# Kernel optimization log

Measured on AMD Instinct MI355X. Metric: run time of the kernel, lower is better.

The kernel has to match this reference:

```python
import jax, jax.numpy as jnp
import numpy as np

D = 128; DFF = 256; NH = 4; HD = D // NH
B = 8; T = 1024
PAIRS = [(0, 1), (1, 2), (0, 2)]  # (ABSTRACT,DYNAMIC),(DYNAMIC,CONCRETE),(ABSTRACT,CONCRETE)
BW = 0.5 / 3.0   # bridge_weight / len(BRIDGE_PAIRS)
LB_W = 0.01


def _hex_np():
    # itertools.product([-1,1], repeat=6): index i = 6-bit binary of i, MSB first, 0->-1
    bits = (np.arange(64)[:, None] >> np.arange(5, -1, -1)) & 1
    return (bits * 2.0 - 1.0).astype(np.float32)


def _anchors_np():
    h = _hex_np()
    idx = {'GEO': 0, 'HYDRO': 18, 'PYRO': 45, 'AERO': 6, 'COSMO': 27, 'NOOS': 63}
    a = (h[idx['NOOS']] + h[idx['COSMO']]) / 2.0   # ABSTRACT
    d = (h[idx['AERO']] + h[idx['PYRO']]) / 2.0    # DYNAMIC
    c = (h[idx['GEO']] + h[idx['HYDRO']]) / 2.0    # CONCRETE
    return np.stack([a, d, c]).astype(np.float32)


def _ln(x, g, b, eps=1e-5):
    m = x.mean(-1, keepdims=True)
    v = ((x - m) ** 2).mean(-1, keepdims=True)
    return (x - m) * jax.lax.rsqrt(v + eps) * g + b


def _mha(q, kv, in_w, out_w):
    # torch nn.MultiheadAttention, bias=False, batch_first
    Bq, Tq, _ = q.shape
    wq, wk, wv = in_w[:D], in_w[D:2 * D], in_w[2 * D:]
    Q = (q @ wq.T).reshape(Bq, Tq, NH, HD)
    K = (kv @ wk.T).reshape(Bq, Tq, NH, HD)
    V = (kv @ wv.T).reshape(Bq, Tq, NH, HD)
    scores = jnp.einsum('bqhd,bkhd->bhqk', Q, K) / jnp.sqrt(jnp.float32(HD))
    attn = jax.nn.softmax(scores, axis=-1)
    o = jnp.einsum('bhqk,bkhd->bqhd', attn, V).reshape(Bq, Tq, D)
    return o @ out_w.T


def setup_inputs() -> dict:
    key = jax.random.key(0)
    ks = iter(jax.random.split(key, 40))
    r = lambda shape, s=0.02: jax.random.normal(next(ks), shape, dtype=jnp.float32) * s
    return {
        'x': jax.random.normal(next(ks), (B, T, D), dtype=jnp.float32),
        'gr_norm_g': jnp.ones((D,), jnp.float32), 'gr_norm_b': jnp.zeros((D,), jnp.float32),
        'q6_w': r((6, D), 0.1),
        'log_temp': jnp.log(jnp.float32(0.5)),
        'grp_norm_g': jnp.ones((3, D), jnp.float32), 'grp_norm_b': jnp.zeros((3, D), jnp.float32),
        'grp_proj_w': r((3, 2, D), 0.1), 'grp_proj_b': jnp.zeros((3, 2), jnp.float32),
        'me_norm_g': jnp.ones((6, D), jnp.float32), 'me_norm_b': jnp.zeros((6, D), jnp.float32),
        'me_gate_w': r((6, DFF, D)), 'me_val_w': r((6, DFF, D)), 'me_out_w': r((6, D, DFF)),
        'br_in_w': r((3, 3 * D, D)), 'br_out_w': r((3, D, D)),
        'br_nq_g': jnp.ones((3, D), jnp.float32), 'br_nq_b': jnp.zeros((3, D), jnp.float32),
        'br_nkv_g': jnp.ones((3, D), jnp.float32), 'br_nkv_b': jnp.zeros((3, D), jnp.float32),
        'br_nffn_g': jnp.ones((3, D), jnp.float32), 'br_nffn_b': jnp.zeros((3, D), jnp.float32),
        'br_gate_w': r((3, 2 * D, D)), 'br_val_w': r((3, 2 * D, D)), 'br_ffn_out_w': r((3, D, 2 * D)),
        'br_gate': jnp.full((3,), -2.0, dtype=jnp.float32),
        'out_norm_g': jnp.ones((D,), jnp.float32), 'out_norm_b': jnp.zeros((D,), jnp.float32),
        'out_w': r((D, D)),
    }


def reference(x, gr_norm_g, gr_norm_b, q6_w, log_temp, grp_norm_g, grp_norm_b,
              grp_proj_w, grp_proj_b, me_norm_g, me_norm_b, me_gate_w, me_val_w,
              me_out_w, br_in_w, br_out_w, br_nq_g, br_nq_b, br_nkv_g, br_nkv_b,
              br_nffn_g, br_nffn_b, br_gate_w, br_val_w, br_ffn_out_w, br_gate,
              out_norm_g, out_norm_b, out_w):
    hexg = jnp.asarray(_hex_np())        # (64, 6)
    anchors = jnp.asarray(_anchors_np())  # (3, 6)

    # ---- GlobalRouter ----
    h = _ln(x, gr_norm_g, gr_norm_b)
    soft_bits = jnp.tanh(h @ q6_w.T)                       # (B,T,6)
    sim = soft_bits @ hexg.T                               # (B,T,64)
    temp = jnp.clip(jnp.exp(log_temp), 0.1, 5.0)
    hex_w = jax.nn.softmax(sim / temp, axis=-1)
    soft_hex = hex_w @ hexg                                # (B,T,6)
    group_weights = jax.nn.softmax(soft_hex @ anchors.T, axis=-1)  # (B,T,3)
    mw = group_weights.mean(axis=(0, 1))
    lb_total = -(mw * jnp.log(mw + 1e-8)).sum()

    # ---- all 6 micro experts (per-expert LayerNorm shares x's stats) ----
    m = x.mean(-1, keepdims=True)
    v = ((x - m) ** 2).mean(-1, keepdims=True)
    xn = (x - m) * jax.lax.rsqrt(v + 1e-5)                 # (B,T,D)
    hme = xn[None] * me_norm_g[:, None, None, :] + me_norm_b[:, None, None, :]  # (6,B,T,D)
    gate = jax.nn.silu(jnp.einsum('ebtd,efd->ebtf', hme, me_gate_w))
    val = jnp.einsum('ebtd,efd->ebtf', hme, me_val_w)
    eo = jnp.einsum('ebtf,edf->ebtd', gate * val, me_out_w)  # (6,B,T,D)

    # ---- per-group routing (2 experts each, top_k=2) ----
    group_outs = []
    for g in range(3):  # groups ordered [ABSTRACT, DYNAMIC, CONCRETE]; experts [2g, 2g+1]
        hg = xn * grp_norm_g[g] + grp_norm_b[g]
        logits = hg @ grp_proj_w[g].T + grp_proj_b[g]      # (B,T,2)
        w = jax.nn.softmax(logits, axis=-1)
        vals, idx = jax.lax.top_k(w, 2)                    # k = min(top_k=2, n=2)
        sparse = (jax.nn.one_hot(idx, 2, dtype=w.dtype) * vals[..., None]).sum(-2)
        sparse = sparse / (sparse.sum(-1, keepdims=True) + 1e-8)
        mwg = w.mean(axis=(0, 1))
        lb_total = lb_total - (mwg * jnp.log(mwg + 1e-8)).sum()
        go = sparse[..., 0:1] * eo[2 * g] + sparse[..., 1:2] * eo[2 * g + 1]
        group_outs.append(group_weights[..., g:g + 1] * go)

    # ---- bridge experts ----
    bridge_sum = jnp.zeros_like(x)
    for i, (a, b) in enumerate(PAIRS):
        xq, xk = group_outs[a], group_outs[b]
        qn = _ln(xq, br_nq_g[i], br_nq_b[i])
        kvn = _ln(xk, br_nkv_g[i], br_nkv_b[i])
        xb = xq + _mha(qn, kvn, br_in_w[i], br_out_w[i])
        hb = _ln(xb, br_nffn_g[i], br_nffn_b[i])
        ff = (jax.nn.silu(hb @ br_gate_w[i].T) * (hb @ br_val_w[i].T)) @ br_ffn_out_w[i].T
        xb = (xb + ff) * jax.nn.sigmoid(br_gate[i])
        bridge_sum = bridge_sum + BW * xb

    combined = group_outs[0] + group_outs[1] + group_outs[2] + bridge_sum
    out = _ln(combined, out_norm_g, out_norm_b) @ out_w.T
    return out, lb_total * LB_W
```

## Files before the change

kernel.cpp:

```cpp
#include <hip/hip_runtime.h>
#include <math.h>

#define DD    128
#define DFF   256
#define NHH   4
#define HDD   32
#define BB    8
#define TT    1024
#define NTOK  (BB*TT)
#define LDK   72
#define QKVN  384

#define WB_MEGATE 0
#define WB_MEVAL  196608
#define WB_MEOUT  393216
#define WB_BRIN   589824
#define WB_BROUT  737280
#define WB_BRG    786432
#define WB_BRV    884736
#define WB_BRF    983040
#define WB_OUTW   1081344
#define WB_TOT    1097728

typedef __bf16 bf16x8 __attribute__((ext_vector_type(8)));
typedef float  f32x4  __attribute__((ext_vector_type(4)));

__device__ __forceinline__ float wsum(float v){
#pragma unroll
  for(int o=32;o>0;o>>=1) v += __shfl_xor(v,o,64);
  return v;
}
__device__ __forceinline__ float wmaxr(float v){
#pragma unroll
  for(int o=32;o>0;o>>=1) v = fmaxf(v,__shfl_xor(v,o,64));
  return v;
}
__device__ __forceinline__ unsigned short f2bf(float x){
  __bf16 h = (__bf16)x;
  unsigned short u;
  __builtin_memcpy(&u, &h, 2);
  return u;
}

__device__ __forceinline__ void stage16(const float* __restrict__ gp,
                                        unsigned short* __restrict__ dst){
  float4 f0 = *reinterpret_cast<const float4*>(gp);
  float4 f1 = *reinterpret_cast<const float4*>(gp+4);
  float4 f2 = *reinterpret_cast<const float4*>(gp+8);
  float4 f3 = *reinterpret_cast<const float4*>(gp+12);
  float f[16] = {f0.x,f0.y,f0.z,f0.w, f1.x,f1.y,f1.z,f1.w,
                 f2.x,f2.y,f2.z,f2.w, f3.x,f3.y,f3.z,f3.w};
  unsigned short h[16];
#pragma unroll
  for(int j=0;j<16;j++) h[j] = f2bf(f[j]);
  *reinterpret_cast<uint4*>(dst)   = *reinterpret_cast<const uint4*>(h);
  *reinterpret_cast<uint4*>(dst+8) = *reinterpret_cast<const uint4*>(h+8);
}

__device__ __forceinline__ void stage16bf(const unsigned short* __restrict__ gp,
                                          unsigned short* __restrict__ dst){
  const uint4* s = reinterpret_cast<const uint4*>(gp);
  *reinterpret_cast<uint4*>(dst)   = s[0];
  *reinterpret_cast<uint4*>(dst+8) = s[1];
}

__device__ __forceinline__ void stageLN(const float* __restrict__ fr,
                                        float mean, float rstd,
                                        const float* __restrict__ g,
                                        const float* __restrict__ b,
                                        unsigned short* __restrict__ dst){
  unsigned short h[16];
#pragma unroll
  for(int j=0;j<16;j++){
    float y = (fr[j]-mean)*rstd*g[j] + b[j];
    h[j] = f2bf(y);
  }
  *reinterpret_cast<uint4*>(dst)   = *reinterpret_cast<const uint4*>(h);
  *reinterpret_cast<uint4*>(dst+8) = *reinterpret_cast<const uint4*>(h+8);
}

__global__ __launch_bounds__(256) void wconv(
    const float* __restrict__ a0, const float* __restrict__ a1, const float* __restrict__ a2,
    const float* __restrict__ a3, const float* __restrict__ a4, const float* __restrict__ a5,
    const float* __restrict__ a6, const float* __restrict__ a7, const float* __restrict__ a8,
    unsigned short* __restrict__ dst, float qsc){
  size_t i = ((size_t)blockIdx.x*256 + threadIdx.x)*4;
  if(i >= WB_TOT) return;
  const float* s; size_t off = i; float sc = 1.0f;
  if(i < WB_MEVAL){ s=a0; }
  else if(i < WB_MEOUT){ s=a1; off = i-WB_MEVAL; }
  else if(i < WB_BRIN ){ s=a2; off = i-WB_MEOUT; }
  else if(i < WB_BROUT){ s=a3; off = i-WB_BRIN;
    int row = (int)(off>>7); if((row % 384) < 128) sc = qsc; }
  else if(i < WB_BRG ){ s=a4; off = i-WB_BROUT; }
  else if(i < WB_BRV ){ s=a5; off = i-WB_BRG; }
  else if(i < WB_BRF ){ s=a6; off = i-WB_BRV; }
  else if(i < WB_OUTW){ s=a7; off = i-WB_BRF; }
  else { s=a8; off = i-WB_OUTW; }
  float4 v = *reinterpret_cast<const float4*>(s + off);
  unsigned short h4[4] = {f2bf(v.x*sc), f2bf(v.y*sc), f2bf(v.z*sc), f2bf(v.w*sc)};
  *reinterpret_cast<uint2*>(dst + i) = *reinterpret_cast<const uint2*>(h4);
}

__global__ __launch_bounds__(256) void routing_kernel(
    const float* __restrict__ x,
    const float* __restrict__ gr_g, const float* __restrict__ gr_b,
    const float* __restrict__ q6,   const float* __restrict__ logtemp,
    const float* __restrict__ grp_g,const float* __restrict__ grp_b,
    const float* __restrict__ gpw,  const float* __restrict__ gpb,
    float* __restrict__ gw_out, float* __restrict__ coef, float* __restrict__ part){
  __shared__ float sp[4][9];
  int lane = threadIdx.x & 63;
  int wv   = threadIdx.x >> 6;
  int t    = (blockIdx.x<<2) + wv;
  const float* xr = x + (size_t)t*DD;
  float r0 = xr[lane], r1 = xr[lane+64];
  float mn = wsum(r0+r1) * (1.0f/DD);
  float d0 = r0-mn, d1 = r1-mn;
  float vv = wsum(d0*d0 + d1*d1) * (1.0f/DD);
  float rstd = rsqrtf(vv + 1e-5f);
  float x0 = d0*rstd, x1 = d1*rstd;
  float h0 = x0*gr_g[lane]+gr_b[lane];
  float h1 = x1*gr_g[lane+64]+gr_b[lane+64];
  float sb[6];
#pragma unroll
  for(int j=0;j<6;j++){
    float p = h0*q6[j*DD+lane] + h1*q6[j*DD+lane+64];
    sb[j] = tanhf(wsum(p));
  }
  float sim = 0.f;
#pragma unroll
  for(int j=0;j<6;j++) sim += ((lane>>(5-j))&1) ? sb[j] : -sb[j];
  float temp = expf(logtemp[0]); temp = fminf(fmaxf(temp,0.1f),5.0f);
  float mx = wmaxr(sim);
  float p  = expf((sim-mx)/temp);
  float w  = p / wsum(p);
  float sh[6];
#pragma unroll
  for(int j=0;j<6;j++) sh[j] = wsum(((lane>>(5-j))&1) ? w : -w);
  const float A0[6]={0,1,1,0,1,1}, A1[6]={0,-1,0,1,0,0}, A2[6]={-1,0,-1,-1,0,-1};
  float l0=0,l1=0,l2=0;
#pragma unroll
  for(int j=0;j<6;j++){ l0+=sh[j]*A0[j]; l1+=sh[j]*A1[j]; l2+=sh[j]*A2[j]; }
  float m3 = fmaxf(l0,fmaxf(l1,l2));
  float e0=expf(l0-m3), e1=expf(l1-m3), e2=expf(l2-m3);
  float inv3 = 1.0f/(e0+e1+e2);
  float g0=e0*inv3, g1=e1*inv3, g2=e2*inv3;
  if(lane==0){ gw_out[t*3]=g0; gw_out[t*3+1]=g1; gw_out[t*3+2]=g2; }
  float gwv[3]={g0,g1,g2};
  float pw[6];
#pragma unroll
  for(int g=0; g<3; g++){
    float hg0 = x0*grp_g[g*DD+lane]    + grp_b[g*DD+lane];
    float hg1 = x1*grp_g[g*DD+lane+64] + grp_b[g*DD+lane+64];
    float q0 = wsum(hg0*gpw[(g*2+0)*DD+lane] + hg1*gpw[(g*2+0)*DD+lane+64]) + gpb[g*2+0];
    float q1 = wsum(hg0*gpw[(g*2+1)*DD+lane] + hg1*gpw[(g*2+1)*DD+lane+64]) + gpb[g*2+1];
    float mm = fmaxf(q0,q1);
    float a0 = expf(q0-mm), a1 = expf(q1-mm);
    float inv = 1.0f/(a0+a1);
    float w0 = a0*inv, w1 = a1*inv;
    pw[g*2]=w0; pw[g*2+1]=w1;
    float invs = 1.0f/(w0+w1+1e-8f);
    if(lane==0){
      coef[(size_t)(2*g  )*NTOK + t] = gwv[g]*w0*invs;
      coef[(size_t)(2*g+1)*NTOK + t] = gwv[g]*w1*invs;
    }
  }
  if(lane==0){
    sp[wv][0]=g0; sp[wv][1]=g1; sp[wv][2]=g2;
#pragma unroll
    for(int k=0;k<6;k++) sp[wv][3+k]=pw[k];
  }
  __syncthreads();
  if(threadIdx.x<9){
    part[blockIdx.x*9+threadIdx.x] =
      sp[0][threadIdx.x]+sp[1][threadIdx.x]+sp[2][threadIdx.x]+sp[3][threadIdx.x];
  }
}

__global__ __launch_bounds__(256) void lb_kernel(const float* __restrict__ part, float* __restrict__ outlb){
  __shared__ float sm[4][9];
  float acc[9] = {};
  for(int i=threadIdx.x; i<2048; i+=256){
#pragma unroll
    for(int c=0;c<9;c++) acc[c] += part[i*9+c];
  }
#pragma unroll
  for(int c=0;c<9;c++) acc[c] = wsum(acc[c]);
  int wv = threadIdx.x>>6, lane = threadIdx.x&63;
  if(lane==0){
#pragma unroll
    for(int c=0;c<9;c++) sm[wv][c]=acc[c];
  }
  __syncthreads();
  if(threadIdx.x==0){
    const float invN = 1.0f/(float)NTOK;
    float lb=0;
#pragma unroll
    for(int c=0;c<9;c++){
      float s = sm[0][c]+sm[1][c]+sm[2][c]+sm[3][c];
      float mw = s*invN;
      lb -= mw*logf(mw+1e-8f);
    }
    outlb[0] = lb*0.01f;
  }
}

template<int MODE,int LN,int ABF,int OBF,int PSEL,int RSEL,int SUM,int QKV,int MRG>
__global__ __launch_bounds__(256) void gemm_mfma(
    const void* __restrict__ Ap, const unsigned short* __restrict__ W, void* __restrict__ Cp,
    int M, int N, int K,
    const float* __restrict__ sv, const float* __restrict__ bv,
    const float* __restrict__ resid, const float* __restrict__ gptr,
    size_t az, size_t wz, size_t cz, size_t pz, size_t rz, size_t gz){
  __shared__ unsigned short As[64*LDK];
  __shared__ unsigned short Ws[64*LDK];
  const int z = blockIdx.z;
  const float* A = (const float*)Ap;
  const unsigned short* Ab = (const unsigned short*)Ap;
  if(QKV){
    bool isQ = (blockIdx.x < 2);
    int s = isQ ? ((z==1)?1:0) : ((z==0)?1:2);
    A += (size_t)s*NTOK*DD;
    if(!isQ){ sv = resid; bv = gptr; }
  } else if(PSEL==0){ A += z*az; Ab += z*az; }
  else if(PSEL==1){ int s = (z==1)?1:0; A += (size_t)s*NTOK*DD; Ab += (size_t)s*NTOK*DD; }
  else            { int s = (z==0)?1:2; A += (size_t)s*NTOK*DD; Ab += (size_t)s*NTOK*DD; }
  W += z*wz;
  float* C = (float*)Cp + z*cz;
  unsigned short* Cb = (unsigned short*)Cp + z*cz;
  const float* rs = resid;
  if(RSEL==0) rs += z*rz;
  else { int s = (z==1)?1:0; rs += (size_t)s*NTOK*DD; }
  sv += z*pz; bv += z*pz;
  const float* gp2 = gptr + z*gz;
  int tid  = threadIdx.x;
  int m0   = blockIdx.y*64, n0 = blockIdx.x*64;
  int w    = tid>>6, lane = tid&63;
  int wr   = (w>>1)*32, wc = (w&1)*32;
  int r    = tid>>2, seg = (tid&3)*16;
  f32x4 acc[2][2] = {};
  auto step = [&](){
#pragma unroll
    for(int kk=0;kk<64;kk+=32){
      int ko = kk + (lane>>4)*8;
      bf16x8 a0 = *reinterpret_cast<const bf16x8*>(&As[(wr    + (lane&15))*LDK + ko]);
      bf16x8 a1 = *reinterpret_cast<const bf16x8*>(&As[(wr+16 + (lane&15))*LDK + ko]);
      bf16x8 b0 = *reinterpret_cast<const bf16x8*>(&Ws[(wc    + (lane&15))*LDK + ko]);
      bf16x8 b1 = *reinterpret_cast<const bf16x8*>(&Ws[(wc+16 + (lane&15))*LDK + ko]);
      acc[0][0] = __builtin_amdgcn_mfma_f32_16x16x32_bf16(a0,b0,acc[0][0],0,0,0);
      acc[0][1] = __builtin_amdgcn_mfma_f32_16x16x32_bf16(a0,b1,acc[0][1],0,0,0);
      acc[1][0] = __builtin_amdgcn_mfma_f32_16x16x32_bf16(a1,b0,acc[1][0],0,0,0);
      acc[1][1] = __builtin_amdgcn_mfma_f32_16x16x32_bf16(a1,b1,acc[1][1],0,0,0);
    }
  };
  if(LN){
    float fr[32]; float mean, rstd;
    if(SUM){
#pragma unroll
      for(int j=0;j<32;j++) fr[j]=0.f;
#pragma unroll
      for(int s=0;s<3;s++){
        const float* r1 = A     + (size_t)s*NTOK*DD + (size_t)(m0+r)*K + seg;
        const float* r2 = resid + (size_t)s*NTOK*DD + (size_t)(m0+r)*K + seg;
#pragma unroll
        for(int j=0;j<4;j++){
          float4 v1 = *reinterpret_cast<const float4*>(r1 + j*4);
          float4 v2 = *reinterpret_cast<const float4*>(r2 + j*4);
          fr[j*4]+=v1.x+v2.x; fr[j*4+1]+=v1.y+v2.y; fr[j*4+2]+=v1.z+v2.z; fr[j*4+3]+=v1.w+v2.w;
          float4 w1 = *reinterpret_cast<const float4*>(r1 + 64 + j*4);
          float4 w2 = *reinterpret_cast<const float4*>(r2 + 64 + j*4);
          fr[16+j*4]+=w1.x+w2.x; fr[16+j*4+1]+=w1.y+w2.y; fr[16+j*4+2]+=w1.z+w2.z; fr[16+j*4+3]+=w1.w+w2.w;
        }
      }
    } else {
      const float* arow = A + (size_t)(m0+r)*K + seg;
#pragma unroll
      for(int j=0;j<4;j++) *reinterpret_cast<float4*>(&fr[j*4])    = *reinterpret_cast<const float4*>(arow + j*4);
#pragma unroll
      for(int j=0;j<4;j++) *reinterpret_cast<float4*>(&fr[16+j*4]) = *reinterpret_cast<const float4*>(arow + 64 + j*4);
    }
    float s1=0.f, s2=0.f;
#pragma unroll
    for(int j=0;j<32;j++){ s1 += fr[j]; s2 += fr[j]*fr[j]; }
    s1 += __shfl_xor(s1,1,64); s1 += __shfl_xor(s1,2,64);
    s2 += __shfl_xor(s2,1,64); s2 += __shfl_xor(s2,2,64);
    mean = s1*(1.0f/DD);
    float var = s2*(1.0f/DD) - mean*mean;
    rstd = rsqrtf(var + 1e-5f);
#pragma unroll
    for(int kh=0; kh<2; ++kh){
      __syncthreads();
      stageLN(fr + kh*16, mean, rstd, sv + kh*64 + seg, bv + kh*64 + seg, &As[r*LDK + seg]);
      stage16bf(W + (size_t)(n0+r)*K + kh*64 + seg, &Ws[r*LDK + seg]);
      __syncthreads();
      step();
    }
  } else if(MRG){
    const float* op0 = (const float*)Ap + (size_t)(2*z)*NTOK*DD;
    const float* op1 = op0 + (size_t)NTOK*DD;
    const float* mp = sv + (size_t)(2*z)*NTOK*NHH;
    const float* lp = bv + (size_t)(2*z)*NTOK*NHH;
    const int row = m0 + r;
#pragma unroll
    for(int kh=0; kh<2; ++kh){
      const int k0 = kh*64;
      const int hh = (k0+seg)>>5;
      size_t ix = (size_t)row*NHH + hh;
      float ma=mp[ix], mb2=mp[(size_t)NTOK*NHH+ix];
      float la=lp[ix], lb2=lp[(size_t)NTOK*NHH+ix];
      float Mx = fmaxf(ma,mb2);
      float f0 = __builtin_amdgcn_exp2f(ma-Mx), f1 = __builtin_amdgcn_exp2f(mb2-Mx);
      float inv = 1.0f/(la*f0+lb2*f1);
      f0 *= inv; f1 *= inv;
      __syncthreads();
      {
        unsigned short hbuf[16];
        size_t base = (size_t)row*DD + k0 + seg;
#pragma unroll
        for(int j=0;j<4;j++){
          float4 v0 = *reinterpret_cast<const float4*>(op0 + base + j*4);
          float4 v1 = *reinterpret_cast<const float4*>(op1 + base + j*4);
          hbuf[j*4  ] = f2bf(v0.x*f0 + v1.x*f1);
          hbuf[j*4+1] = f2bf(v0.y*f0 + v1.y*f1);
          hbuf[j*4+2] = f2bf(v0.z*f0 + v1.z*f1);
          hbuf[j*4+3] = f2bf(v0.w*f0 + v1.w*f1);
        }
        *reinterpret_cast<uint4*>(&As[r*LDK+seg])   = *reinterpret_cast<const uint4*>(hbuf);
        *reinterpret_cast<uint4*>(&As[r*LDK+seg+8]) = *reinterpret_cast<const uint4*>(hbuf+8);
      }
      stage16bf(W + (size_t)(n0+r)*K + k0 + seg, &Ws[r*LDK + seg]);
      __syncthreads();
      step();
    }
  } else {
    for(int k0=0;k0<K;k0+=64){
      __syncthreads();
      if(ABF) stage16bf(Ab + (size_t)(m0+r)*K + k0 + seg, &As[r*LDK + seg]);
      else    stage16(A  + (size_t)(m0+r)*K + k0 + seg, &As[r*LDK + seg]);
      stage16bf(W + (size_t)(n0+r)*K + k0 + seg, &Ws[r*LDK + seg]);
      __syncthreads();
      step();
    }
  }
#pragma unroll
  for(int i=0;i<2;i++){
#pragma unroll
    for(int j=0;j<2;j++){
      int mb = m0 + wr + i*16 + (lane>>4)*4;
      int n  = n0 + wc + j*16 + (lane&15);
#pragma unroll
      for(int rg=0;rg<4;rg++){
        int m = mb + rg;
        float v = acc[i][j][rg];
        size_t o = (size_t)m*N + n;
        if(MODE==0){ if(OBF) Cb[o] = f2bf(v); else C[o] = v; }
        else if(MODE==3){ C[o] = rs[o] + v; }
        else if(MODE==5){
          float gs = (0.5f/3.0f)/(1.0f+expf(-gp2[0]));
          C[o] = gs*(rs[o]+v);
        }
      }
    }
  }
}

__global__ __launch_bounds__(256) void gemm_dual(
    const float* __restrict__ A, const unsigned short* __restrict__ G,
    const unsigned short* __restrict__ V,
    unsigned short* __restrict__ C, int M, int N, int K,
    const float* __restrict__ sv, const float* __restrict__ bv,
    size_t az, size_t wz, size_t cz, size_t pz){
  __shared__ unsigned short As[64*LDK];
  __shared__ unsigned short Gs[64*LDK];
  __shared__ unsigned short Vs[64*LDK];
  const int z = blockIdx.z;
  A += z*az; G += z*wz; V += z*wz; C += z*cz; sv += z*pz; bv += z*pz;
  int tid  = threadIdx.x;
  int m0   = blockIdx.y*64, n0 = blockIdx.x*64;
  int w    = tid>>6, lane = tid&63;
  int wr   = (w>>1)*32, wc = (w&1)*32;
  int r    = tid>>2, seg = (tid&3)*16;
  f32x4 accg[2][2] = {};
  f32x4 accv[2][2] = {};
  float fr[32]; float mean, rstd;
  {
    const float* arow = A + (size_t)(m0+r)*K + seg;
#pragma unroll
    for(int j=0;j<4;j++) *reinterpret_cast<float4*>(&fr[j*4])    = *reinterpret_cast<const float4*>(arow + j*4);
#pragma unroll
    for(int j=0;j<4;j++) *reinterpret_cast<float4*>(&fr[16+j*4]) = *reinterpret_cast<const float4*>(arow + 64 + j*4);
    float s1=0.f, s2=0.f;
#pragma unroll
    for(int j=0;j<32;j++){ s1 += fr[j]; s2 += fr[j]*fr[j]; }
    s1 += __shfl_xor(s1,1,64); s1 += __shfl_xor(s1,2,64);
    s2 += __shfl_xor(s2,1,64); s2 += __shfl_xor(s2,2,64);
    mean = s1*(1.0f/DD);
    float var = s2*(1.0f/DD) - mean*mean;
    rstd = rsqrtf(var + 1e-5f);
  }
#pragma unroll
  for(int kh=0; kh<2; ++kh){
    int k0 = kh*64;
    __syncthreads();
    stageLN(fr + kh*16, mean, rstd, sv + k0 + seg, bv + k0 + seg, &As[r*LDK + seg]);
    stage16bf(G + (size_t)(n0+r)*K + k0 + seg, &Gs[r*LDK + seg]);
    stage16bf(V + (size_t)(n0+r)*K + k0 + seg, &Vs[r*LDK + seg]);
    __syncthreads();
#pragma unroll
    for(int kk=0;kk<64;kk+=32){
      int ko = kk + (lane>>4)*8;
      bf16x8 a0 = *reinterpret_cast<const bf16x8*>(&As[(wr    + (lane&15))*LDK + ko]);
      bf16x8 a1 = *reinterpret_cast<const bf16x8*>(&As[(wr+16 + (lane&15))*LDK + ko]);
      bf16x8 g0 = *reinterpret_cast<const bf16x8*>(&Gs[(wc    + (lane&15))*LDK + ko]);
      bf16x8 g1 = *reinterpret_cast<const bf16x8*>(&Gs[(wc+16 + (lane&15))*LDK + ko]);
      bf16x8 v0 = *reinterpret_cast<const bf16x8*>(&Vs[(wc    + (lane&15))*LDK + ko]);
      bf16x8 v1 = *reinterpret_cast<const bf16x8*>(&Vs[(wc+16 + (lane&15))*LDK + ko]);
      accg[0][0] = __builtin_amdgcn_mfma_f32_16x16x32_bf16(a0,g0,accg[0][0],0,0,0);
      accg[0][1] = __builtin_amdgcn_mfma_f32_16x16x32_bf16(a0,g1,accg[0][1],0,0,0);
      accg[1][0] = __builtin_amdgcn_mfma_f32_16x16x32_bf16(a1,g0,accg[1][0],0,0,0);
      accg[1][1] = __builtin_amdgcn_mfma_f32_16x16x32_bf16(a1,g1,accg[1][1],0,0,0);
      accv[0][0] = __builtin_amdgcn_mfma_f32_16x16x32_bf16(a0,v0,accv[0][0],0,0,0);
      accv[0][1] = __builtin_amdgcn_mfma_f32_16x16x32_bf16(a0,v1,accv[0][1],0,0,0);
      accv[1][0] = __builtin_amdgcn_mfma_f32_16x16x32_bf16(a1,v0,accv[1][0],0,0,0);
      accv[1][1] = __builtin_amdgcn_mfma_f32_16x16x32_bf16(a1,v1,accv[1][1],0,0,0);
    }
  }
#pragma unroll
  for(int i=0;i<2;i++){
#pragma unroll
    for(int j=0;j<2;j++){
      int mb = m0 + wr + i*16 + (lane>>4)*4;
      int n  = n0 + wc + j*16 + (lane&15);
#pragma unroll
      for(int rg=0;rg<4;rg++){
        float gg = accg[i][j][rg];
        float vv = accv[i][j][rg];
        float sg = gg/(1.0f+expf(-gg));
        C[(size_t)(mb+rg)*N + n] = f2bf(sg*vv);
      }
    }
  }
}

__global__ __launch_bounds__(256) void gemm_moe2(
    const unsigned short* __restrict__ Ab, const unsigned short* __restrict__ Wb,
    float* __restrict__ Cb, const float* __restrict__ coef){
  __shared__ unsigned short As0[64*LDK];
  __shared__ unsigned short As1[64*LDK];
  __shared__ unsigned short Ws0[64*LDK];
  __shared__ unsigned short Ws1[64*LDK];
  const int g = blockIdx.z;
  const unsigned short* A0 = Ab + (size_t)(2*g)*NTOK*DFF;
  const unsigned short* A1 = A0 + (size_t)NTOK*DFF;
  const unsigned short* W0 = Wb + (size_t)(2*g)*DD*DFF;
  const unsigned short* W1 = W0 + (size_t)DD*DFF;
  float* C = Cb + (size_t)g*NTOK*DD;
  const float* c0 = coef + (size_t)(2*g)*NTOK;
  const float* c1 = c0 + NTOK;
  int tid  = threadIdx.x;
  int m0   = blockIdx.y*64, n0 = blockIdx.x*64;
  int w    = tid>>6, lane = tid&63;
  int wr   = (w>>1)*32, wc = (w&1)*32;
  int r    = tid>>2, seg = (tid&3)*16;
  f32x4 a0acc[2][2] = {};
  f32x4 a1acc[2][2] = {};
  for(int k0=0;k0<DFF;k0+=64){
    __syncthreads();
    stage16bf(A0 + (size_t)(m0+r)*DFF + k0 + seg, &As0[r*LDK + seg]);
    stage16bf(A1 + (size_t)(m0+r)*DFF + k0 + seg, &As1[r*LDK + seg]);
    stage16bf(W0 + (size_t)(n0+r)*DFF + k0 + seg, &Ws0[r*LDK + seg]);
    stage16bf(W1 + (size_t)(n0+r)*DFF + k0 + seg, &Ws1[r*LDK + seg]);
    __syncthreads();
#pragma unroll
    for(int kk=0;kk<64;kk+=32){
      int ko = kk + (lane>>4)*8;
      bf16x8 x00 = *reinterpret_cast<const bf16x8*>(&As0[(wr    + (lane&15))*LDK + ko]);
      bf16x8 x01 = *reinterpret_cast<const bf16x8*>(&As0[(wr+16 + (lane&15))*LDK + ko]);
      bf16x8 x10 = *reinterpret_cast<const bf16x8*>(&As1[(wr    + (lane&15))*LDK + ko]);
      bf16x8 x11 = *reinterpret_cast<const bf16x8*>(&As1[(wr+16 + (lane&15))*LDK + ko]);
      bf16x8 w00 = *reinterpret_cast<const bf16x8*>(&Ws0[(wc    + (lane&15))*LDK + ko]);
      bf16x8 w01 = *reinterpret_cast<const bf16x8*>(&Ws0[(wc+16 + (lane&15))*LDK + ko]);
      bf16x8 w10 = *reinterpret_cast<const bf16x8*>(&Ws1[(wc    + (lane&15))*LDK + ko]);
      bf16x8 w11 = *reinterpret_cast<const bf16x8*>(&Ws1[(wc+16 + (lane&15))*LDK + ko]);
      a0acc[0][0] = __builtin_amdgcn_mfma_f32_16x16x32_bf16(x00,w00,a0acc[0][0],0,0,0);
      a0acc[0][1] = __builtin_amdgcn_mfma_f32_16x16x32_bf16(x00,w01,a0acc[0][1],0,0,0);
      a0acc[1][0] = __builtin_amdgcn_mfma_f32_16x16x32_bf16(x01,w00,a0acc[1][0],0,0,0);
      a0acc[1][1] = __builtin_amdgcn_mfma_f32_16x16x32_bf16(x01,w01,a0acc[1][1],0,0,0);
      a1acc[0][0] = __builtin_amdgcn_mfma_f32_16x16x32_bf16(x10,w10,a1acc[0][0],0,0,0);
      a1acc[0][1] = __builtin_amdgcn_mfma_f32_16x16x32_bf16(x10,w11,a1acc[0][1],0,0,0);
      a1acc[1][0] = __builtin_amdgcn_mfma_f32_16x16x32_bf16(x11,w10,a1acc[1][0],0,0,0);
      a1acc[1][1] = __builtin_amdgcn_mfma_f32_16x16x32_bf16(x11,w11,a1acc[1][1],0,0,0);
    }
  }
#pragma unroll
  for(int i=0;i<2;i++){
#pragma unroll
    for(int j=0;j<2;j++){
      int mb = m0 + wr + i*16 + (lane>>4)*4;
      int n  = n0 + wc + j*16 + (lane&15);
#pragma unroll
      for(int rg=0;rg<4;rg++){
        int m = mb + rg;
        C[(size_t)m*DD + n] = c0[m]*a0acc[i][j][rg] + c1[m]*a1acc[i][j][rg];
      }
    }
  }
}

#define PSW(row) (((row)&8)<<1)
#define VSW(row) ((((row)>>3)&3)<<3)
__global__ __launch_bounds__(256) void attn_split(
    const unsigned short* __restrict__ qkv,
    float* __restrict__ opart, float* __restrict__ mpart, float* __restrict__ lpart){
  __shared__ __align__(16) unsigned short Ks[64*40];
  __shared__ __align__(16) unsigned short Vt[48*72];
  __shared__ __align__(16) unsigned short Ps[4][16*72];
  const int tid = threadIdx.x;
  const int w = tid>>6, lane = tid&63;
  const int lr = lane&15, lg = lane>>4;
  const int bx = blockIdx.x & 15, sp = blockIdx.x >> 4;
  const int h = blockIdx.y;
  const int b = blockIdx.z & 7, br = blockIdx.z >> 3;
  const int qtok0 = b*TT + bx*64 + w*16;
  for(int idx=tid; idx<16*72; idx+=256)
    Vt[32*72 + idx] = (idx < 64) ? (unsigned short)0x3F80 : (unsigned short)0;
  const unsigned short* qp = qkv + (size_t)br*NTOK*QKVN + (size_t)(qtok0 + lr)*QKVN + h*HDD + lg*8;
  bf16x8 qa = *reinterpret_cast<const bf16x8*>(qp);
  f32x4 o0 = {}, o1 = {}, o2 = {};
  float m[4] = {-1e30f,-1e30f,-1e30f,-1e30f};
  const unsigned short* KVbase = qkv + (size_t)br*NTOK*QKVN + (size_t)(b*TT)*QKVN + DD + h*HDD;
  const int sp2 = br*2 + sp;

  for(int t0=sp*(TT/2); t0<(sp+1)*(TT/2); t0+=64){
    __syncthreads();
#pragma unroll
    for(int s2=0;s2<2;s2++){
      int i   = tid + s2*256;
      int key = i>>3, seg = (i&7)*4;
      const unsigned short* src = KVbase + (size_t)(t0+key)*QKVN + seg;
      *reinterpret_cast<uint2*>(&Ks[key*40+seg]) = *reinterpret_cast<const uint2*>(src);
      unsigned short vs[4];
      *reinterpret_cast<uint2*>(vs) = *reinterpret_cast<const uint2*>(src + DD);
      const int kc = key ^ VSW(seg);
      Vt[(seg  )*72+kc] = vs[0];
      Vt[(seg+1)*72+kc] = vs[1];
      Vt[(seg+2)*72+kc] = vs[2];
      Vt[(seg+3)*72+kc] = vs[3];
    }
    __syncthreads();
    f32x4 s[4];
#pragma unroll
    for(int f=0;f<4;f++){
      bf16x8 kb = *reinterpret_cast<const bf16x8*>(&Ks[(f*16+lr)*40 + lg*8]);
      f32x4 z = {};
      s[f] = __builtin_amdgcn_mfma_f32_16x16x32_bf16(qa,kb,z,0,0,0);
    }
    float tmax[4]; bool need=false;
#pragma unroll
    for(int r=0;r<4;r++){
      tmax[r] = fmaxf(fmaxf(s[0][r],s[1][r]),fmaxf(s[2][r],s[3][r]));
      need = need || (tmax[r] > m[r] + 8.0f);
    }
    if(__any(need)){
#pragma unroll
      for(int r=0;r<4;r++){
        float t = tmax[r];
#pragma unroll
        for(int off=1;off<16;off<<=1) t = fmaxf(t,__shfl_xor(t,off,64));
        float nm = fmaxf(m[r],t);
        float sc = __builtin_amdgcn_exp2f(m[r]-nm);
        m[r] = nm; o0[r] *= sc; o1[r] *= sc; o2[r] *= sc;
      }
    }
#pragma unroll
    for(int r=0;r<4;r++){
      const int q = lg*4+r;
      const int cw = PSW(q);
#pragma unroll
      for(int f=0;f<4;f++){
        float p = __builtin_amdgcn_exp2f(s[f][r]-m[r]);
        Ps[w][q*72 + ((f*16+lr)^cw)] = f2bf(p);
      }
    }
    const int pw_ = PSW(lr);
    bf16x8 pa0 = *reinterpret_cast<const bf16x8*>(&Ps[w][lr*72 + ((lg*8   )^pw_)]);
    bf16x8 pa1 = *reinterpret_cast<const bf16x8*>(&Ps[w][lr*72 + ((lg*8+32)^pw_)]);
    {
      const int r_ = lr, vw = VSW(r_);
      bf16x8 vb0 = *reinterpret_cast<const bf16x8*>(&Vt[r_*72 + ((lg*8   )^vw)]);
      bf16x8 vb1 = *reinterpret_cast<const bf16x8*>(&Vt[r_*72 + ((lg*8+32)^vw)]);
      o0 = __builtin_amdgcn_mfma_f32_16x16x32_bf16(pa0,vb0,o0,0,0,0);
      o0 = __builtin_amdgcn_mfma_f32_16x16x32_bf16(pa1,vb1,o0,0,0,0);
    }
    {
      const int r_ = 16+lr, vw = VSW(r_);
      bf16x8 vb0 = *reinterpret_cast<const bf16x8*>(&Vt[r_*72 + ((lg*8   )^vw)]);
      bf16x8 vb1 = *reinterpret_cast<const bf16x8*>(&Vt[r_*72 + ((lg*8+32)^vw)]);
      o1 = __builtin_amdgcn_mfma_f32_16x16x32_bf16(pa0,vb0,o1,0,0,0);
      o1 = __builtin_amdgcn_mfma_f32_16x16x32_bf16(pa1,vb1,o1,0,0,0);
    }
    {
      const int r_ = 32+lr, vw = VSW(r_);
      bf16x8 vb0 = *reinterpret_cast<const bf16x8*>(&Vt[r_*72 + ((lg*8   )^vw)]);
      bf16x8 vb1 = *reinterpret_cast<const bf16x8*>(&Vt[r_*72 + ((lg*8+32)^vw)]);
      o2 = __builtin_amdgcn_mfma_f32_16x16x32_bf16(pa0,vb0,o2,0,0,0);
      o2 = __builtin_amdgcn_mfma_f32_16x16x32_bf16(pa1,vb1,o2,0,0,0);
    }
  }
#pragma unroll
  for(int r=0;r<4;r++){
    float lsr = __shfl(o2[r], lane & 48, 64);
    int row = qtok0 + lg*4 + r;
    float* op = opart + ((size_t)sp2*NTOK + row)*DD + h*HDD;
    op[lr]    = o0[r];
    op[16+lr] = o1[r];
    if(lr==0){
      mpart[((size_t)sp2*NTOK+row)*NHH + h] = m[r];
      lpart[((size_t)sp2*NTOK+row)*NHH + h] = lsr;
    }
  }
}

extern "C" void kernel_launch(void* const* d_in, const int* in_sizes, int n_in,
                              void* d_out, int out_size, void* d_ws, size_t ws_size,
                              hipStream_t stream){
  (void)in_sizes; (void)n_in; (void)out_size; (void)ws_size;
  const float* x       = (const float*)d_in[0];
  const float* gr_g    = (const float*)d_in[1];
  const float* gr_b    = (const float*)d_in[2];
  const float* q6_w    = (const float*)d_in[3];
  const float* logtemp = (const float*)d_in[4];
  const float* grp_g   = (const float*)d_in[5];
  const float* grp_b   = (const float*)d_in[6];
  const float* gpw     = (const float*)d_in[7];
  const float* gpb     = (const float*)d_in[8];
  const float* me_g    = (const float*)d_in[9];
  const float* me_b    = (const float*)d_in[10];
  const float* me_gate = (const float*)d_in[11];
  const float* me_val  = (const float*)d_in[12];
  const float* me_out  = (const float*)d_in[13];
  const float* br_in   = (const float*)d_in[14];
  const float* br_outw = (const float*)d_in[15];
  const float* nq_g    = (const float*)d_in[16];
  const float* nq_b    = (const float*)d_in[17];
  const float* nkv_g   = (const float*)d_in[18];
  const float* nkv_b   = (const float*)d_in[19];
  const float* nff_g   = (const float*)d_in[20];
  const float* nff_b   = (const float*)d_in[21];
  const float* brg_w   = (const float*)d_in[22];
  const float* brv_w   = (const float*)d_in[23];
  const float* brf_w   = (const float*)d_in[24];
  const float* br_gate = (const float*)d_in[25];
  const float* on_g    = (const float*)d_in[26];
  const float* on_b    = (const float*)d_in[27];
  const float* out_w   = (const float*)d_in[28];
  float* out = (float*)d_out;
  float* ws  = (float*)d_ws;

  float* coef  = ws;
  float* part  = ws + 65536;
  unsigned short* gvb6 = (unsigned short*)(ws + 131072);
  float* go    = ws + 6731072;
  unsigned short* qkv  = (unsigned short*)(ws + 9900000);
  float* opart = ws + 14700000;
  float* mpart = ws + 21000000;
  float* lpart = ws + 21200000;
  unsigned short* wbf  = (unsigned short*)(ws + 21400000);
  float* xb    = ws + 23000000;
  unsigned short* gvb2 = (unsigned short*)(ws + 26200000);
  float* bsum  = ws + 29400000;
  float* gw    = ws + 32700000;

  const float qscale = 0.17677669529663687f * 1.4426950408889634f;

  wconv<<<1072,256,0,stream>>>(me_gate, me_val, me_out, br_in, br_outw,
                               brg_w, brv_w, brf_w, out_w, wbf, qscale);

  routing_kernel<<<2048,256,0,stream>>>(x, gr_g, gr_b, q6_w, logtemp,
                                        grp_g, grp_b, gpw, gpb, gw, coef, part);
  lb_kernel<<<1,256,0,stream>>>(part, out + 1048576);

  gemm_dual<<<dim3(4,128,6),256,0,stream>>>(x, wbf+WB_MEGATE, wbf+WB_MEVAL, gvb6,
      NTOK,DFF,DD, me_g, me_b, 0, (size_t)DFF*DD, (size_t)NTOK*DFF, DD);
  gemm_moe2<<<dim3(2,128,3),256,0,stream>>>(gvb6, wbf+WB_MEOUT, go, coef);

  gemm_mfma<0,1,0,1,0,0,0,1,0><<<dim3(6,128,3),256,0,stream>>>(go, wbf+WB_BRIN, qkv,
      NTOK,QKVN,DD, nq_g, nq_b, nkv_g, nkv_b,
      0, (size_t)QKVN*DD, (size_t)NTOK*QKVN, DD, 0, 0);
  attn_split<<<dim3(32,NHH,24),256,0,stream>>>(qkv, opart, mpart, lpart);
  gemm_mfma<3,0,0,0,0,1,0,0,1><<<dim3(2,128,3),256,0,stream>>>(opart, wbf+WB_BROUT, xb,
      NTOK,DD,DD, mpart, lpart, go, nullptr,
      0, (size_t)DD*DD, (size_t)NTOK*DD, 0, 0, 0);
  gemm_dual<<<dim3(4,128,3),256,0,stream>>>(xb, wbf+WB_BRG, wbf+WB_BRV, gvb2,
      NTOK,2*DD,DD, nff_g, nff_b, (size_t)NTOK*DD, (size_t)2*DD*DD, (size_t)NTOK*2*DD, DD);
  gemm_mfma<5,0,1,0,0,0,0,0,0><<<dim3(2,128,3),256,0,stream>>>(gvb2, wbf+WB_BRF, bsum,
      NTOK,DD,2*DD, nullptr, nullptr, xb, br_gate,
      (size_t)NTOK*2*DD, (size_t)DD*2*DD, (size_t)NTOK*DD, 0, (size_t)NTOK*DD, 1);

  gemm_mfma<0,1,0,0,0,0,1,0,0><<<dim3(2,128,1),256,0,stream>>>(go, wbf+WB_OUTW, out,
      NTOK,DD,DD, on_g, on_b, bsum, nullptr,
      0, 0, 0, 0, 0, 0);
}
```

Measured before the change: 198.2 us.

## Replace split-KV attention with single-pass attention writing normalized bf16 output

```diff
diff --git a/kernel.cpp b/kernel.cpp
--- a/kernel.cpp
+++ b/kernel.cpp
@@ -206,7 +206,7 @@
   }
 }
 
-template<int MODE,int LN,int ABF,int OBF,int PSEL,int RSEL,int SUM,int QKV,int MRG>
+template<int MODE,int LN,int ABF,int OBF,int PSEL,int RSEL,int SUM,int QKV>
 __global__ __launch_bounds__(256) void gemm_mfma(
     const void* __restrict__ Ap, const unsigned short* __restrict__ W, void* __restrict__ Cp,
     int M, int N, int K,
@@ -296,43 +296,6 @@
       __syncthreads();
       step();
     }
-  } else if(MRG){
-    const float* op0 = (const float*)Ap + (size_t)(2*z)*NTOK*DD;
-    const float* op1 = op0 + (size_t)NTOK*DD;
-    const float* mp = sv + (size_t)(2*z)*NTOK*NHH;
-    const float* lp = bv + (size_t)(2*z)*NTOK*NHH;
-    const int row = m0 + r;
-#pragma unroll
-    for(int kh=0; kh<2; ++kh){
-      const int k0 = kh*64;
-      const int hh = (k0+seg)>>5;
-      size_t ix = (size_t)row*NHH + hh;
-      float ma=mp[ix], mb2=mp[(size_t)NTOK*NHH+ix];
-      float la=lp[ix], lb2=lp[(size_t)NTOK*NHH+ix];
-      float Mx = fmaxf(ma,mb2);
-      float f0 = __builtin_amdgcn_exp2f(ma-Mx), f1 = __builtin_amdgcn_exp2f(mb2-Mx);
-      float inv = 1.0f/(la*f0+lb2*f1);
-      f0 *= inv; f1 *= inv;
-      __syncthreads();
-      {
-        unsigned short hbuf[16];
-        size_t base = (size_t)row*DD + k0 + seg;
-#pragma unroll
-        for(int j=0;j<4;j++){
-          float4 v0 = *reinterpret_cast<const float4*>(op0 + base + j*4);
-          float4 v1 = *reinterpret_cast<const float4*>(op1 + base + j*4);
-          hbuf[j*4  ] = f2bf(v0.x*f0 + v1.x*f1);
-          hbuf[j*4+1] = f2bf(v0.y*f0 + v1.y*f1);
-          hbuf[j*4+2] = f2bf(v0.z*f0 + v1.z*f1);
-          hbuf[j*4+3] = f2bf(v0.w*f0 + v1.w*f1);
-        }
-        *reinterpret_cast<uint4*>(&As[r*LDK+seg])   = *reinterpret_cast<const uint4*>(hbuf);
-        *reinterpret_cast<uint4*>(&As[r*LDK+seg+8]) = *reinterpret_cast<const uint4*>(hbuf+8);
-      }
-      stage16bf(W + (size_t)(n0+r)*K + k0 + seg, &Ws[r*LDK + seg]);
-      __syncthreads();
-      step();
-    }
   } else {
     for(int k0=0;k0<K;k0+=64){
       __syncthreads();
@@ -510,16 +473,16 @@
 
 #define PSW(row) (((row)&8)<<1)
 #define VSW(row) ((((row)>>3)&3)<<3)
-__global__ __launch_bounds__(256) void attn_split(
+__global__ __launch_bounds__(256) void attn_fused(
     const unsigned short* __restrict__ qkv,
-    float* __restrict__ opart, float* __restrict__ mpart, float* __restrict__ lpart){
+    unsigned short* __restrict__ obuf){
   __shared__ __align__(16) unsigned short Ks[64*40];
   __shared__ __align__(16) unsigned short Vt[48*72];
   __shared__ __align__(16) unsigned short Ps[4][16*72];
   const int tid = threadIdx.x;
   const int w = tid>>6, lane = tid&63;
   const int lr = lane&15, lg = lane>>4;
-  const int bx = blockIdx.x & 15, sp = blockIdx.x >> 4;
+  const int bx = blockIdx.x;
   const int h = blockIdx.y;
   const int b = blockIdx.z & 7, br = blockIdx.z >> 3;
   const int qtok0 = b*TT + bx*64 + w*16;
@@ -530,9 +493,8 @@
   f32x4 o0 = {}, o1 = {}, o2 = {};
   float m[4] = {-1e30f,-1e30f,-1e30f,-1e30f};
   const unsigned short* KVbase = qkv + (size_t)br*NTOK*QKVN + (size_t)(b*TT)*QKVN + DD + h*HDD;
-  const int sp2 = br*2 + sp;
-
-  for(int t0=sp*(TT/2); t0<(sp+1)*(TT/2); t0+=64){
+
+  for(int t0=0; t0<TT; t0+=64){
     __syncthreads();
 #pragma unroll
     for(int s2=0;s2<2;s2++){
@@ -611,14 +573,11 @@
 #pragma unroll
   for(int r=0;r<4;r++){
     float lsr = __shfl(o2[r], lane & 48, 64);
+    float inv = 1.0f/lsr;
     int row = qtok0 + lg*4 + r;
-    float* op = opart + ((size_t)sp2*NTOK + row)*DD + h*HDD;
-    op[lr]    = o0[r];
-    op[16+lr] = o1[r];
-    if(lr==0){
-      mpart[((size_t)sp2*NTOK+row)*NHH + h] = m[r];
-      lpart[((size_t)sp2*NTOK+row)*NHH + h] = lsr;
-    }
+    unsigned short* orow = obuf + (size_t)br*NTOK*DD + (size_t)row*DD + h*HDD;
+    orow[lr]    = f2bf(o0[r]*inv);
+    orow[16+lr] = f2bf(o1[r]*inv);
   }
 }
 
@@ -663,9 +622,7 @@
   unsigned short* gvb6 = (unsigned short*)(ws + 131072);
   float* go    = ws + 6731072;
   unsigned short* qkv  = (unsigned short*)(ws + 9900000);
-  float* opart = ws + 14700000;
-  float* mpart = ws + 21000000;
-  float* lpart = ws + 21200000;
+  unsigned short* obuf = (unsigned short*)(ws + 14700000);
   unsigned short* wbf  = (unsigned short*)(ws + 21400000);
   float* xb    = ws + 23000000;
   unsigned short* gvb2 = (unsigned short*)(ws + 26200000);
@@ -685,20 +642,20 @@
       NTOK,DFF,DD, me_g, me_b, 0, (size_t)DFF*DD, (size_t)NTOK*DFF, DD);
   gemm_moe2<<<dim3(2,128,3),256,0,stream>>>(gvb6, wbf+WB_MEOUT, go, coef);
 
-  gemm_mfma<0,1,0,1,0,0,0,1,0><<<dim3(6,128,3),256,0,stream>>>(go, wbf+WB_BRIN, qkv,
+  gemm_mfma<0,1,0,1,0,0,0,1><<<dim3(6,128,3),256,0,stream>>>(go, wbf+WB_BRIN, qkv,
       NTOK,QKVN,DD, nq_g, nq_b, nkv_g, nkv_b,
       0, (size_t)QKVN*DD, (size_t)NTOK*QKVN, DD, 0, 0);
-  attn_split<<<dim3(32,NHH,24),256,0,stream>>>(qkv, opart, mpart, lpart);
-  gemm_mfma<3,0,0,0,0,1,0,0,1><<<dim3(2,128,3),256,0,stream>>>(opart, wbf+WB_BROUT, xb,
-      NTOK,DD,DD, mpart, lpart, go, nullptr,
-      0, (size_t)DD*DD, (size_t)NTOK*DD, 0, 0, 0);
+  attn_fused<<<dim3(16,NHH,24),256,0,stream>>>(qkv, obuf);
+  gemm_mfma<3,0,1,0,0,1,0,0><<<dim3(2,128,3),256,0,stream>>>(obuf, wbf+WB_BROUT, xb,
+      NTOK,DD,DD, nullptr, nullptr, go, nullptr,
+      (size_t)NTOK*DD, (size_t)DD*DD, (size_t)NTOK*DD, 0, 0, 0);
   gemm_dual<<<dim3(4,128,3),256,0,stream>>>(xb, wbf+WB_BRG, wbf+WB_BRV, gvb2,
       NTOK,2*DD,DD, nff_g, nff_b, (size_t)NTOK*DD, (size_t)2*DD*DD, (size_t)NTOK*2*DD, DD);
-  gemm_mfma<5,0,1,0,0,0,0,0,0><<<dim3(2,128,3),256,0,stream>>>(gvb2, wbf+WB_BRF, bsum,
+  gemm_mfma<5,0,1,0,0,0,0,0><<<dim3(2,128,3),256,0,stream>>>(gvb2, wbf+WB_BRF, bsum,
       NTOK,DD,2*DD, nullptr, nullptr, xb, br_gate,
       (size_t)NTOK*2*DD, (size_t)DD*2*DD, (size_t)NTOK*DD, 0, (size_t)NTOK*DD, 1);
 
-  gemm_mfma<0,1,0,0,0,0,1,0,0><<<dim3(2,128,1),256,0,stream>>>(go, wbf+WB_OUTW, out,
+  gemm_mfma<0,1,0,0,0,0,1,0><<<dim3(2,128,1),256,0,stream>>>(go, wbf+WB_OUTW, out,
       NTOK,DD,DD, on_g, on_b, bsum, nullptr,
       0, 0, 0, 0, 0, 0);
 }
```

Result: faster. 194.3 us (-2.0%).
